# Performance work log

Hardware: AMD Instinct MI355X
Metric: run time of the kernel (lower is better)

## Reference

```python
import jax, jax.numpy as jnp
import numpy as np

DIM = 1024
HEADS = 16
DIM_HEAD = 64
INNER = HEADS * DIM_HEAD  # 1024
EPS = 1e-5


def setup_inputs() -> dict:
    key = jax.random.key(0)
    ks = jax.random.split(key, 8)
    B, N = 4, 2048
    s = 0.02
    return {
        "query": jax.random.normal(ks[0], (B, N, DIM), jnp.float32),
        "key_": jax.random.normal(ks[1], (B, N, DIM), jnp.float32),
        "value": jax.random.normal(ks[2], (B, N, DIM), jnp.float32),
        "Wq": jax.random.normal(ks[3], (DIM, INNER), jnp.float32) * s,
        "Wk": jax.random.normal(ks[4], (DIM, INNER), jnp.float32) * s,
        "Wv": jax.random.normal(ks[5], (DIM, INNER), jnp.float32) * s,
        "Wo": jax.random.normal(ks[6], (INNER, DIM), jnp.float32) * s,
        "bo": jnp.zeros((DIM,), jnp.float32),
        "gamma": jnp.ones((DIM,), jnp.float32),
        "beta": jnp.zeros((DIM,), jnp.float32),
    }


def reference(query, key_, value, Wq, Wk, Wv, Wo, bo, gamma, beta):
    B, N, _ = query.shape
    scale = DIM_HEAD ** (-0.5)
    # project and split heads: [B, H, N, Dh]
    q = (query @ Wq).reshape(B, N, HEADS, DIM_HEAD).transpose(0, 2, 1, 3)
    k = (key_ @ Wk).reshape(B, N, HEADS, DIM_HEAD).transpose(0, 2, 1, 3)
    v = (value @ Wv).reshape(B, N, HEADS, DIM_HEAD).transpose(0, 2, 1, 3)
    dots = jnp.einsum("bhnd,bhmd->bhnm", q, k) * scale  # [B,H,N,N]
    attn = jax.nn.softmax(dots, axis=-1)
    out = jnp.einsum("bhnm,bhmd->bhnd", attn, v)
    out = out.transpose(0, 2, 1, 3).reshape(B, N, INNER)
    out = out @ Wo + bo  # dropout p=0.0 is identity
    # LayerNorm over last dim
    mu = out.mean(-1, keepdims=True)
    var = ((out - mu) ** 2).mean(-1, keepdims=True)
    normed = (out - mu) * jax.lax.rsqrt(var + EPS) * gamma + beta
    return normed + query
```

## Files before the change

kernel.cpp:

```cpp
#include <hip/hip_runtime.h>
#include <stdint.h>

#define K_DIM 1024
#define B_SZ 4
#define N_SEQ 2048
#define HEADS 16
#define DH 64
#define M_TOT (B_SZ * N_SEQ)

typedef __bf16 bf16x8 __attribute__((ext_vector_type(8)));
typedef __bf16 bf16x4 __attribute__((ext_vector_type(4)));
typedef float f32x4 __attribute__((ext_vector_type(4)));
typedef short s16x4 __attribute__((ext_vector_type(4)));

typedef const uint32_t __attribute__((address_space(1))) gas_u32;
typedef uint32_t __attribute__((address_space(3))) las_u32;

#define CE_SCALE 0.1803368801f

__device__ __forceinline__ uint16_t f2bf(float f) {
  uint32_t u = __float_as_uint(f);
  u += 0x7FFFu + ((u >> 16) & 1u);
  return (uint16_t)(u >> 16);
}

__device__ __forceinline__ void gld_lds16(const uint16_t* g, uint16_t* lds) {
  __builtin_amdgcn_global_load_lds((gas_u32*)g, (las_u32*)lds, 16, 0, 0);
}

#if defined(__has_builtin)
#if __has_builtin(__builtin_amdgcn_mfma_f32_16x16x16bf16_1k)
#define HAVE_MFMA16_BUILTIN 1
#endif
#endif

__device__ __forceinline__ f32x4 mfma16(bf16x4 a, bf16x4 b, f32x4 c) {
#ifdef HAVE_MFMA16_BUILTIN
  return __builtin_amdgcn_mfma_f32_16x16x16bf16_1k(
      __builtin_bit_cast(s16x4, a), __builtin_bit_cast(s16x4, b), c, 0, 0, 0);
#else
  f32x4 d;
  asm("v_mfma_f32_16x16x16_bf16 %0, %1, %2, %3"
      : "=v"(d)
      : "v"(a), "v"(b), "v"(c));
  return d;
#endif
}

__global__ __launch_bounds__(256) void conv_bf16_k(const float* __restrict__ s0,
                                                   const float* __restrict__ s1,
                                                   const float* __restrict__ s2,
                                                   uint16_t* __restrict__ dstbase, int n4) {
  const int z = blockIdx.y;
  const float* src = (z == 0) ? s0 : (z == 1) ? s1 : s2;
  uint16_t* dst = dstbase + (size_t)z * M_TOT * K_DIM;
  int i = blockIdx.x * blockDim.x + threadIdx.x;
  if (i < n4) {
    float4 v = ((const float4*)src)[i];
    ushort4 o;
    o.x = f2bf(v.x); o.y = f2bf(v.y); o.z = f2bf(v.z); o.w = f2bf(v.w);
    ((ushort4*)dst)[i] = o;
  }
}

__global__ __launch_bounds__(256) void transpose_conv(const float* __restrict__ s0,
                                                      const float* __restrict__ s1,
                                                      const float* __restrict__ s2,
                                                      const float* __restrict__ s3,
                                                      uint16_t* __restrict__ dstbase) {
  __shared__ float tile[32][33];
  const int z = blockIdx.z;
  const float* src = (z == 0) ? s0 : (z == 1) ? s1 : (z == 2) ? s2 : s3;
  uint16_t* dst = dstbase + (size_t)z * 1024 * 1024;
  const int tx = threadIdx.x, ty = threadIdx.y;
  const int bx = blockIdx.x * 32, by = blockIdx.y * 32;
#pragma unroll
  for (int i = 0; i < 32; i += 8)
    tile[ty + i][tx] = src[(size_t)(by + ty + i) * 1024 + bx + tx];
  __syncthreads();
#pragma unroll
  for (int i = 0; i < 32; i += 8)
    dst[(size_t)(bx + ty + i) * 1024 + by + tx] = f2bf(tile[tx][ty + i]);
}

template <int MODE>
__global__ __launch_bounds__(256, 2) void gemm_bf16(const uint16_t* __restrict__ A,
                                                    const uint16_t* __restrict__ BT,
                                                    void* __restrict__ Cout,
                                                    const float* __restrict__ bias) {
  __shared__ __align__(16) uint16_t As[128 * 32];
  __shared__ __align__(16) uint16_t Bs[128 * 32];
  const int tid = threadIdx.x;
  const int wave = tid >> 6, lane = tid & 63;
  const int g = lane >> 4, c16 = lane & 15;

  const int bid = blockIdx.x;
  const int xcd = bid & 7;
  const int l = bid >> 3;
  const int z = (MODE == 3) ? (l >> 6) : 0;
  const int r = l & 63;
  const int n0 = (r & 7) * 128;
  const int m0 = (xcd * 8 + (r >> 3)) * 128;

  const int wr = wave >> 1, wc = wave & 1;
  float scale = 1.f;
  if (MODE == 3) {
    A += (size_t)z * M_TOT * K_DIM;
    BT += (size_t)z * 1024 * 1024;
    scale = (z == 0) ? CE_SCALE : 1.f;
  }

  const f32x4 fzero = {0.f, 0.f, 0.f, 0.f};
  f32x4 acc[4][4];
#pragma unroll
  for (int i = 0; i < 4; ++i)
#pragma unroll
    for (int j = 0; j < 4; ++j) acc[i][j] = fzero;

  const int srow = wave * 32 + (lane >> 2);
  const int scol = (lane & 3) * 8;
  const uint16_t* ag0 = A + (size_t)(m0 + srow) * K_DIM + scol;
  const uint16_t* ag1 = A + (size_t)(m0 + srow + 16) * K_DIM + scol;
  const uint16_t* bg0 = BT + (size_t)(n0 + srow) * K_DIM + scol;
  const uint16_t* bg1 = BT + (size_t)(n0 + srow + 16) * K_DIM + scol;
  uint16_t* la0 = &As[(wave * 32) * 32];
  uint16_t* la1 = &As[(wave * 32 + 16) * 32];
  uint16_t* lb0 = &Bs[(wave * 32) * 32];
  uint16_t* lb1 = &Bs[(wave * 32 + 16) * 32];

  for (int kt = 0; kt < K_DIM / 32; ++kt) {
    __syncthreads();
    gld_lds16(ag0 + kt * 32, la0);
    gld_lds16(ag1 + kt * 32, la1);
    gld_lds16(bg0 + kt * 32, lb0);
    gld_lds16(bg1 + kt * 32, lb1);
    __syncthreads();
    bf16x8 avec[4], bvec[4];
#pragma unroll
    for (int i = 0; i < 4; ++i)
      avec[i] = *(const bf16x8*)&As[(wr * 64 + i * 16 + c16) * 32 + g * 8];
#pragma unroll
    for (int j = 0; j < 4; ++j)
      bvec[j] = *(const bf16x8*)&Bs[(wc * 64 + j * 16 + c16) * 32 + g * 8];
#pragma unroll
    for (int i = 0; i < 4; ++i)
#pragma unroll
      for (int j = 0; j < 4; ++j)
        acc[i][j] = __builtin_amdgcn_mfma_f32_16x16x32_bf16(avec[i], bvec[j], acc[i][j], 0, 0, 0);
  }

#pragma unroll
  for (int i = 0; i < 4; ++i) {
#pragma unroll
    for (int j = 0; j < 4; ++j) {
      const int col = n0 + wc * 64 + j * 16 + c16;
      if (MODE == 3 && z == 2) {
        const int h = col >> 6, d = col & 63;
        const int row0 = m0 + wr * 64 + i * 16 + g * 4;
        const int b = row0 >> 11, n = row0 & 2047;
        ushort4 o;
        o.x = f2bf(acc[i][j][0]); o.y = f2bf(acc[i][j][1]);
        o.z = f2bf(acc[i][j][2]); o.w = f2bf(acc[i][j][3]);
        *(ushort4*)&((uint16_t*)Cout)[(size_t)2 * M_TOT * 1024 +
                                      (((size_t)(b * HEADS + h)) * DH + d) * N_SEQ + n] = o;
      } else {
#pragma unroll
        for (int r2 = 0; r2 < 4; ++r2) {
          const int row = m0 + wr * 64 + i * 16 + g * 4 + r2;
          if (MODE == 3) {
            const int b = row >> 11, n = row & 2047;
            const int h = col >> 6, d = col & 63;
            ((uint16_t*)Cout)[(size_t)z * M_TOT * 1024 +
                              (((size_t)(b * HEADS + h)) * N_SEQ + n) * DH + d] =
                f2bf(acc[i][j][r2] * scale);
          } else {
            ((float*)Cout)[(size_t)row * 1024 + col] = acc[i][j][r2] + bias[col];
          }
        }
      }
    }
  }
}

__global__ __launch_bounds__(256, 2) void attention_k(const uint16_t* __restrict__ qm,
                                                      const uint16_t* __restrict__ km,
                                                      const uint16_t* __restrict__ vtm,
                                                      uint16_t* __restrict__ om) {
  __shared__ __align__(16) uint16_t Ks[64 * 64];
  __shared__ __align__(16) uint16_t Vs[64 * 64];
  const int tid = threadIdx.x;
  const int wave = tid >> 6, lane = tid & 63;
  const int g = lane >> 4, c16 = lane & 15;

  const int bid = blockIdx.x;
  const int xcd = bid & 7;
  const int l0 = bid >> 3;
  const int bh = xcd * 8 + (l0 & 7);
  const int qblk = l0 >> 3;
  const int b = bh >> 4, h = bh & 15;
  const int q0 = qblk * 256 + wave * 64;

  const uint16_t* qbase = qm + (size_t)bh * N_SEQ * DH;
  const uint16_t* kbase = km + (size_t)bh * N_SEQ * DH;
  const uint16_t* vbase = vtm + (size_t)bh * DH * N_SEQ;

  bf16x8 qf[4][2];
#pragma unroll
  for (int qc = 0; qc < 4; ++qc) {
    const uint16_t* qp = qbase + (size_t)(q0 + qc * 16 + c16) * DH + g * 8;
    qf[qc][0] = *(const bf16x8*)qp;
    qf[qc][1] = *(const bf16x8*)(qp + 32);
  }

  const f32x4 fz = {0.f, 0.f, 0.f, 0.f};
  f32x4 oacc[4][4];
#pragma unroll
  for (int qc = 0; qc < 4; ++qc)
#pragma unroll
    for (int jt = 0; jt < 4; ++jt) oacc[qc][jt] = fz;
  float l[4] = {0.f, 0.f, 0.f, 0.f};

  const int sw = c16 & 7;

  const int ch = tid & 7;
  const int krow0 = tid >> 3, krow1 = (256 + tid) >> 3;
  const int kdst0 = krow0 * 64 + ((ch ^ (krow0 & 7)) << 3);
  const int kdst1 = krow1 * 64 + ((ch ^ (krow1 & 7)) << 3);

  uint4 kp0, kp1, vp0, vp1;
  kp0 = *(const uint4*)&kbase[(size_t)tid * 8];
  kp1 = *(const uint4*)&kbase[(size_t)(256 + tid) * 8];
  vp0 = *(const uint4*)&vbase[(size_t)krow0 * N_SEQ + ch * 8];
  vp1 = *(const uint4*)&vbase[(size_t)krow1 * N_SEQ + ch * 8];
  *(uint4*)&Ks[kdst0] = kp0;
  *(uint4*)&Ks[kdst1] = kp1;
  *(uint4*)&Vs[kdst0] = vp0;
  *(uint4*)&Vs[kdst1] = vp1;
  __syncthreads();

  for (int t = 0; t < N_SEQ / 64; ++t) {
    if (t < N_SEQ / 64 - 1) {
      const size_t ko = (size_t)(t + 1) * 4096;
      const int vc = (t + 1) * 64;
      kp0 = *(const uint4*)&kbase[ko + (size_t)tid * 8];
      kp1 = *(const uint4*)&kbase[ko + (size_t)(256 + tid) * 8];
      vp0 = *(const uint4*)&vbase[(size_t)krow0 * N_SEQ + vc + ch * 8];
      vp1 = *(const uint4*)&vbase[(size_t)krow1 * N_SEQ + vc + ch * 8];
    }

#pragma unroll
    for (int kt = 0; kt < 4; ++kt) {
      const int krow = kt * 16 + c16;
      bf16x8 kf0 = *(const bf16x8*)&Ks[krow * 64 + ((g ^ sw) << 3)];
      bf16x8 kf1 = *(const bf16x8*)&Ks[krow * 64 + (((4 + g) ^ sw) << 3)];
      bf16x4 pk[4];
#pragma unroll
      for (int qc = 0; qc < 4; ++qc) {
        f32x4 z = fz;
        z = __builtin_amdgcn_mfma_f32_16x16x32_bf16(kf0, qf[qc][0], z, 0, 0, 0);
        z = __builtin_amdgcn_mfma_f32_16x16x32_bf16(kf1, qf[qc][1], z, 0, 0, 0);
        const float p0 = __builtin_amdgcn_exp2f(z[0]);
        const float p1 = __builtin_amdgcn_exp2f(z[1]);
        const float p2 = __builtin_amdgcn_exp2f(z[2]);
        const float p3 = __builtin_amdgcn_exp2f(z[3]);
        l[qc] += (p0 + p1) + (p2 + p3);
        bf16x4 pq;
        pq[0] = (__bf16)p0; pq[1] = (__bf16)p1; pq[2] = (__bf16)p2; pq[3] = (__bf16)p3;
        pk[qc] = pq;
      }
#pragma unroll
      for (int jt = 0; jt < 4; ++jt) {
        bf16x4 vb = *(const bf16x4*)&Vs[(jt * 16 + c16) * 64 +
                                        (((kt * 2 + (g >> 1)) ^ sw) << 3) + (g & 1) * 4];
#pragma unroll
        for (int qc = 0; qc < 4; ++qc) oacc[qc][jt] = mfma16(pk[qc], vb, oacc[qc][jt]);
      }
    }

    if (t < N_SEQ / 64 - 1) {
      __syncthreads();
      *(uint4*)&Ks[kdst0] = kp0;
      *(uint4*)&Ks[kdst1] = kp1;
      *(uint4*)&Vs[kdst0] = vp0;
      *(uint4*)&Vs[kdst1] = vp1;
      __syncthreads();
    }
  }

#pragma unroll
  for (int qc = 0; qc < 4; ++qc) {
    l[qc] += __shfl_xor(l[qc], 16);
    l[qc] += __shfl_xor(l[qc], 32);
  }

#pragma unroll
  for (int qc = 0; qc < 4; ++qc) {
#pragma unroll
    for (int r = 0; r < 4; ++r) {
      const float lr = __shfl(l[qc], g * 4 + r, 16);
      const float inv = 1.f / lr;
      const int row = q0 + qc * 16 + g * 4 + r;
      const size_t base = ((size_t)b * N_SEQ + row) * 1024 + h * 64;
#pragma unroll
      for (int jt = 0; jt < 4; ++jt)
        om[base + jt * 16 + c16] = f2bf(oacc[qc][jt][r] * inv);
    }
  }
}

__global__ __launch_bounds__(256) void ln_res_k(const float* __restrict__ proj,
                                                const float* __restrict__ query,
                                                const float* __restrict__ gamma,
                                                const float* __restrict__ beta,
                                                float* __restrict__ out) {
  const int row = blockIdx.x;
  const int tid = threadIdx.x;
  const size_t base = (size_t)row * 1024 + tid * 4;
  float4 v = *(const float4*)(proj + base);
  float s = v.x + v.y + v.z + v.w;
  float s2 = v.x * v.x + v.y * v.y + v.z * v.z + v.w * v.w;
#pragma unroll
  for (int off = 1; off < 64; off <<= 1) {
    s += __shfl_xor(s, off);
    s2 += __shfl_xor(s2, off);
  }
  __shared__ float red[8];
  const int wave = tid >> 6, lane = tid & 63;
  if (lane == 0) { red[wave] = s; red[4 + wave] = s2; }
  __syncthreads();
  s = red[0] + red[1] + red[2] + red[3];
  s2 = red[4] + red[5] + red[6] + red[7];
  const float mu = s * (1.f / 1024.f);
  const float var = fmaxf(s2 * (1.f / 1024.f) - mu * mu, 0.f);
  const float rstd = rsqrtf(var + 1e-5f);
  float4 gq = *(const float4*)(gamma + tid * 4);
  float4 bq = *(const float4*)(beta + tid * 4);
  float4 qq = *(const float4*)(query + base);
  float4 o;
  o.x = (v.x - mu) * rstd * gq.x + bq.x + qq.x;
  o.y = (v.y - mu) * rstd * gq.y + bq.y + qq.y;
  o.z = (v.z - mu) * rstd * gq.z + bq.z + qq.z;
  o.w = (v.w - mu) * rstd * gq.w + bq.w + qq.w;
  *(float4*)(out + base) = o;
}

extern "C" void kernel_launch(void* const* d_in, const int* in_sizes, int n_in,
                              void* d_out, int out_size, void* d_ws, size_t ws_size,
                              hipStream_t stream) {
  (void)in_sizes; (void)n_in; (void)out_size; (void)ws_size;
  const float* query = (const float*)d_in[0];
  const float* key_ = (const float*)d_in[1];
  const float* value = (const float*)d_in[2];
  const float* Wq = (const float*)d_in[3];
  const float* Wk = (const float*)d_in[4];
  const float* Wv = (const float*)d_in[5];
  const float* Wo = (const float*)d_in[6];
  const float* bo = (const float*)d_in[7];
  const float* gamma = (const float*)d_in[8];
  const float* beta = (const float*)d_in[9];
  float* out = (float*)d_out;

  const size_t NELEM = (size_t)M_TOT * 1024;
  uint16_t* wsp = (uint16_t*)d_ws;
  uint16_t* WqT = wsp;
  uint16_t* WoT = WqT + 3 * 1024 * 1024;
  uint16_t* xq = WqT + 4 * 1024 * 1024;
  uint16_t* qb = xq + 3 * NELEM;
  uint16_t* attnO = xq;
  float* proj = (float*)(xq + NELEM);

  const int n4 = (int)(NELEM / 4);
  conv_bf16_k<<<dim3(8192, 3), 256, 0, stream>>>(query, key_, value, xq, n4);

  transpose_conv<<<dim3(32, 32, 4), dim3(32, 8), 0, stream>>>(Wq, Wk, Wv, Wo, WqT);

  gemm_bf16<3><<<1536, 256, 0, stream>>>(xq, WqT, qb, nullptr);

  attention_k<<<512, 256, 0, stream>>>(qb, qb + NELEM, qb + 2 * NELEM, attnO);

  gemm_bf16<1><<<512, 256, 0, stream>>>(attnO, WoT, proj, bo);

  ln_res_k<<<8192, 256, 0, stream>>>(proj, query, gamma, beta, out);
}
```

Baseline: 346.1 us.

## Double-buffer K/V tiles and use 8 waves of 32 query rows in attention

The attention kernel now launches 512 threads per block, with each wave handling 32 query rows instead of 64. K/V tiles in shared memory are double-buffered, so each iteration needs one barrier instead of two, and every thread stages a single 16-byte chunk of K and V. The aim is more waves for latency hiding and less synchronisation stall. In exchange each wave holds fewer accumulators, so every K/V LDS fragment feeds half as many MFMAs, and shared-memory use per block doubles.

```diff
diff --git a/kernel.cpp b/kernel.cpp
--- a/kernel.cpp
+++ b/kernel.cpp
@@ -182,12 +182,12 @@
   }
 }
 
-__global__ __launch_bounds__(256, 2) void attention_k(const uint16_t* __restrict__ qm,
+__global__ __launch_bounds__(512, 4) void attention_k(const uint16_t* __restrict__ qm,
                                                       const uint16_t* __restrict__ km,
                                                       const uint16_t* __restrict__ vtm,
                                                       uint16_t* __restrict__ om) {
-  __shared__ __align__(16) uint16_t Ks[64 * 64];
-  __shared__ __align__(16) uint16_t Vs[64 * 64];
+  __shared__ __align__(16) uint16_t Ks[2 * 64 * 64];
+  __shared__ __align__(16) uint16_t Vs[2 * 64 * 64];
   const int tid = threadIdx.x;
   const int wave = tid >> 6, lane = tid & 63;
   const int g = lane >> 4, c16 = lane & 15;
@@ -198,64 +198,61 @@
   const int bh = xcd * 8 + (l0 & 7);
   const int qblk = l0 >> 3;
   const int b = bh >> 4, h = bh & 15;
-  const int q0 = qblk * 256 + wave * 64;
+  const int q0 = qblk * 256 + wave * 32;
 
   const uint16_t* qbase = qm + (size_t)bh * N_SEQ * DH;
   const uint16_t* kbase = km + (size_t)bh * N_SEQ * DH;
   const uint16_t* vbase = vtm + (size_t)bh * DH * N_SEQ;
 
-  bf16x8 qf[4][2];
-#pragma unroll
-  for (int qc = 0; qc < 4; ++qc) {
+  bf16x8 qf[2][2];
+#pragma unroll
+  for (int qc = 0; qc < 2; ++qc) {
     const uint16_t* qp = qbase + (size_t)(q0 + qc * 16 + c16) * DH + g * 8;
     qf[qc][0] = *(const bf16x8*)qp;
     qf[qc][1] = *(const bf16x8*)(qp + 32);
   }
 
   const f32x4 fz = {0.f, 0.f, 0.f, 0.f};
-  f32x4 oacc[4][4];
-#pragma unroll
-  for (int qc = 0; qc < 4; ++qc)
+  f32x4 oacc[2][4];
+#pragma unroll
+  for (int qc = 0; qc < 2; ++qc)
 #pragma unroll
     for (int jt = 0; jt < 4; ++jt) oacc[qc][jt] = fz;
-  float l[4] = {0.f, 0.f, 0.f, 0.f};
+  float l[2] = {0.f, 0.f};
 
   const int sw = c16 & 7;
 
   const int ch = tid & 7;
-  const int krow0 = tid >> 3, krow1 = (256 + tid) >> 3;
-  const int kdst0 = krow0 * 64 + ((ch ^ (krow0 & 7)) << 3);
-  const int kdst1 = krow1 * 64 + ((ch ^ (krow1 & 7)) << 3);
-
-  uint4 kp0, kp1, vp0, vp1;
-  kp0 = *(const uint4*)&kbase[(size_t)tid * 8];
-  kp1 = *(const uint4*)&kbase[(size_t)(256 + tid) * 8];
-  vp0 = *(const uint4*)&vbase[(size_t)krow0 * N_SEQ + ch * 8];
-  vp1 = *(const uint4*)&vbase[(size_t)krow1 * N_SEQ + ch * 8];
-  *(uint4*)&Ks[kdst0] = kp0;
-  *(uint4*)&Ks[kdst1] = kp1;
-  *(uint4*)&Vs[kdst0] = vp0;
-  *(uint4*)&Vs[kdst1] = vp1;
+  const int srow = tid >> 3;
+  const int kdst = srow * 64 + ((ch ^ (srow & 7)) << 3);
+
+  uint4 kp, vp;
+  kp = *(const uint4*)&kbase[(size_t)tid * 8];
+  vp = *(const uint4*)&vbase[(size_t)srow * N_SEQ + ch * 8];
+  *(uint4*)&Ks[kdst] = kp;
+  *(uint4*)&Vs[kdst] = vp;
   __syncthreads();
 
   for (int t = 0; t < N_SEQ / 64; ++t) {
+    const int cur = t & 1;
     if (t < N_SEQ / 64 - 1) {
       const size_t ko = (size_t)(t + 1) * 4096;
       const int vc = (t + 1) * 64;
-      kp0 = *(const uint4*)&kbase[ko + (size_t)tid * 8];
-      kp1 = *(const uint4*)&kbase[ko + (size_t)(256 + tid) * 8];
-      vp0 = *(const uint4*)&vbase[(size_t)krow0 * N_SEQ + vc + ch * 8];
-      vp1 = *(const uint4*)&vbase[(size_t)krow1 * N_SEQ + vc + ch * 8];
-    }
+      kp = *(const uint4*)&kbase[ko + (size_t)tid * 8];
+      vp = *(const uint4*)&vbase[(size_t)srow * N_SEQ + vc + ch * 8];
+    }
+
+    const uint16_t* ks = &Ks[cur * 4096];
+    const uint16_t* vs = &Vs[cur * 4096];
 
 #pragma unroll
     for (int kt = 0; kt < 4; ++kt) {
       const int krow = kt * 16 + c16;
-      bf16x8 kf0 = *(const bf16x8*)&Ks[krow * 64 + ((g ^ sw) << 3)];
-      bf16x8 kf1 = *(const bf16x8*)&Ks[krow * 64 + (((4 + g) ^ sw) << 3)];
-      bf16x4 pk[4];
-#pragma unroll
-      for (int qc = 0; qc < 4; ++qc) {
+      bf16x8 kf0 = *(const bf16x8*)&ks[krow * 64 + ((g ^ sw) << 3)];
+      bf16x8 kf1 = *(const bf16x8*)&ks[krow * 64 + (((4 + g) ^ sw) << 3)];
+      bf16x4 pk[2];
+#pragma unroll
+      for (int qc = 0; qc < 2; ++qc) {
         f32x4 z = fz;
         z = __builtin_amdgcn_mfma_f32_16x16x32_bf16(kf0, qf[qc][0], z, 0, 0, 0);
         z = __builtin_amdgcn_mfma_f32_16x16x32_bf16(kf1, qf[qc][1], z, 0, 0, 0);
@@ -270,31 +267,28 @@
       }
 #pragma unroll
       for (int jt = 0; jt < 4; ++jt) {
-        bf16x4 vb = *(const bf16x4*)&Vs[(jt * 16 + c16) * 64 +
+        bf16x4 vb = *(const bf16x4*)&vs[(jt * 16 + c16) * 64 +
                                         (((kt * 2 + (g >> 1)) ^ sw) << 3) + (g & 1) * 4];
 #pragma unroll
-        for (int qc = 0; qc < 4; ++qc) oacc[qc][jt] = mfma16(pk[qc], vb, oacc[qc][jt]);
+        for (int qc = 0; qc < 2; ++qc) oacc[qc][jt] = mfma16(pk[qc], vb, oacc[qc][jt]);
       }
     }
 
     if (t < N_SEQ / 64 - 1) {
+      *(uint4*)&Ks[(cur ^ 1) * 4096 + kdst] = kp;
+      *(uint4*)&Vs[(cur ^ 1) * 4096 + kdst] = vp;
       __syncthreads();
-      *(uint4*)&Ks[kdst0] = kp0;
-      *(uint4*)&Ks[kdst1] = kp1;
-      *(uint4*)&Vs[kdst0] = vp0;
-      *(uint4*)&Vs[kdst1] = vp1;
-      __syncthreads();
-    }
-  }
-
-#pragma unroll
-  for (int qc = 0; qc < 4; ++qc) {
+    }
+  }
+
+#pragma unroll
+  for (int qc = 0; qc < 2; ++qc) {
     l[qc] += __shfl_xor(l[qc], 16);
     l[qc] += __shfl_xor(l[qc], 32);
   }
 
 #pragma unroll
-  for (int qc = 0; qc < 4; ++qc) {
+  for (int qc = 0; qc < 2; ++qc) {
 #pragma unroll
     for (int r = 0; r < 4; ++r) {
       const float lr = __shfl(l[qc], g * 4 + r, 16);
@@ -376,7 +370,7 @@
 
   gemm_bf16<3><<<1536, 256, 0, stream>>>(xq, WqT, qb, nullptr);
 
-  attention_k<<<512, 256, 0, stream>>>(qb, qb + NELEM, qb + 2 * NELEM, attnO);
+  attention_k<<<512, 512, 0, stream>>>(qb, qb + NELEM, qb + 2 * NELEM, attnO);
 
   gemm_bf16<1><<<512, 256, 0, stream>>>(attnO, WoT, proj, bo);
 
```

After: 348.7 us. Within noise of the previous version (+0.7%).

## Switch attention kernel to 32x32x16 MFMA with permlane-swapped P and double-buffered LDS

Applied to the files above, without the earlier changes.

Restructures the attention inner loop to use 32x32x16 bf16 MFMA tiles for both QK^T and PV. The P fragments are repacked in registers with v_permlane32_swap so they can feed the second MFMA directly. K/V shared-memory tiles are double-buffered, which removes one barrier per iteration, and setprio hints are added around the MFMA bursts. The aim is fewer MFMA and LDS instructions per FLOP and less sync overhead, at the cost of more registers and LDS, which may reduce occupancy.

```diff
diff --git a/kernel.cpp b/kernel.cpp
--- a/kernel.cpp
+++ b/kernel.cpp
@@ -10,8 +10,9 @@
 
 typedef __bf16 bf16x8 __attribute__((ext_vector_type(8)));
 typedef __bf16 bf16x4 __attribute__((ext_vector_type(4)));
+typedef __bf16 bf16x2 __attribute__((ext_vector_type(2)));
 typedef float f32x4 __attribute__((ext_vector_type(4)));
-typedef short s16x4 __attribute__((ext_vector_type(4)));
+typedef float f32x16 __attribute__((ext_vector_type(16)));
 
 typedef const uint32_t __attribute__((address_space(1))) gas_u32;
 typedef uint32_t __attribute__((address_space(3))) las_u32;
@@ -28,23 +29,15 @@
   __builtin_amdgcn_global_load_lds((gas_u32*)g, (las_u32*)lds, 16, 0, 0);
 }
 
-#if defined(__has_builtin)
-#if __has_builtin(__builtin_amdgcn_mfma_f32_16x16x16bf16_1k)
-#define HAVE_MFMA16_BUILTIN 1
-#endif
-#endif
-
-__device__ __forceinline__ f32x4 mfma16(bf16x4 a, bf16x4 b, f32x4 c) {
-#ifdef HAVE_MFMA16_BUILTIN
-  return __builtin_amdgcn_mfma_f32_16x16x16bf16_1k(
-      __builtin_bit_cast(s16x4, a), __builtin_bit_cast(s16x4, b), c, 0, 0, 0);
-#else
-  f32x4 d;
-  asm("v_mfma_f32_16x16x16_bf16 %0, %1, %2, %3"
-      : "=v"(d)
-      : "v"(a), "v"(b), "v"(c));
-  return d;
-#endif
+__device__ __forceinline__ uint32_t pkbf(float a, float b) {
+  bf16x2 t;
+  t[0] = (__bf16)a;
+  t[1] = (__bf16)b;
+  return __builtin_bit_cast(uint32_t, t);
+}
+
+__device__ __forceinline__ void pswap(uint32_t& a, uint32_t& b) {
+  asm("v_permlane32_swap_b32 %0, %1" : "+v"(a), "+v"(b));
 }
 
 __global__ __launch_bounds__(256) void conv_bf16_k(const float* __restrict__ s0,
@@ -186,11 +179,12 @@
                                                       const uint16_t* __restrict__ km,
                                                       const uint16_t* __restrict__ vtm,
                                                       uint16_t* __restrict__ om) {
-  __shared__ __align__(16) uint16_t Ks[64 * 64];
-  __shared__ __align__(16) uint16_t Vs[64 * 64];
+  __shared__ __align__(16) uint16_t Ks[2 * 64 * 64];
+  __shared__ __align__(16) uint16_t Vs[2 * 64 * 64];
   const int tid = threadIdx.x;
   const int wave = tid >> 6, lane = tid & 63;
-  const int g = lane >> 4, c16 = lane & 15;
+  const int lrow = lane & 31;
+  const int hi = lane >> 5;
 
   const int bid = blockIdx.x;
   const int xcd = bid & 7;
@@ -198,32 +192,47 @@
   const int bh = xcd * 8 + (l0 & 7);
   const int qblk = l0 >> 3;
   const int b = bh >> 4, h = bh & 15;
-  const int q0 = qblk * 256 + wave * 64;
+  const int q0w = qblk * 256 + wave * 64;
 
   const uint16_t* qbase = qm + (size_t)bh * N_SEQ * DH;
   const uint16_t* kbase = km + (size_t)bh * N_SEQ * DH;
   const uint16_t* vbase = vtm + (size_t)bh * DH * N_SEQ;
 
-  bf16x8 qf[4][2];
-#pragma unroll
-  for (int qc = 0; qc < 4; ++qc) {
-    const uint16_t* qp = qbase + (size_t)(q0 + qc * 16 + c16) * DH + g * 8;
-    qf[qc][0] = *(const bf16x8*)qp;
-    qf[qc][1] = *(const bf16x8*)(qp + 32);
-  }
-
-  const f32x4 fz = {0.f, 0.f, 0.f, 0.f};
-  f32x4 oacc[4][4];
-#pragma unroll
-  for (int qc = 0; qc < 4; ++qc)
-#pragma unroll
-    for (int jt = 0; jt < 4; ++jt) oacc[qc][jt] = fz;
-  float l[4] = {0.f, 0.f, 0.f, 0.f};
-
-  const int sw = c16 & 7;
+  bf16x8 qf[2][4];
+#pragma unroll
+  for (int qs = 0; qs < 2; ++qs) {
+    const uint16_t* qp = qbase + (size_t)(q0w + qs * 32 + lrow) * DH + hi * 8;
+#pragma unroll
+    for (int step = 0; step < 4; ++step) qf[qs][step] = *(const bf16x8*)(qp + step * 16);
+  }
+
+  int koff[2][4];
+  int voff[2][2][2];
+#pragma unroll
+  for (int ks = 0; ks < 2; ++ks) {
+    const int krow = ks * 32 + lrow;
+#pragma unroll
+    for (int step = 0; step < 4; ++step)
+      koff[ks][step] = krow * 64 + ((((step << 1) | hi) ^ (krow & 7)) << 3);
+#pragma unroll
+    for (int s = 0; s < 2; ++s)
+#pragma unroll
+      for (int dt = 0; dt < 2; ++dt)
+        voff[ks][s][dt] =
+            (dt * 32 + lrow) * 64 + ((((ks << 2) | (s << 1) | hi) ^ (lrow & 7)) << 3);
+  }
+
+  f32x16 oacc[2][2];
+#pragma unroll
+  for (int qs = 0; qs < 2; ++qs)
+#pragma unroll
+    for (int dt = 0; dt < 2; ++dt)
+#pragma unroll
+      for (int i = 0; i < 16; ++i) oacc[qs][dt][i] = 0.f;
+  float l[2] = {0.f, 0.f};
 
   const int ch = tid & 7;
-  const int krow0 = tid >> 3, krow1 = (256 + tid) >> 3;
+  const int krow0 = tid >> 3, krow1 = 32 + (tid >> 3);
   const int kdst0 = krow0 * 64 + ((ch ^ (krow0 & 7)) << 3);
   const int kdst1 = krow1 * 64 + ((ch ^ (krow1 & 7)) << 3);
 
@@ -239,6 +248,7 @@
   __syncthreads();
 
   for (int t = 0; t < N_SEQ / 64; ++t) {
+    const int cur = t & 1;
     if (t < N_SEQ / 64 - 1) {
       const size_t ko = (size_t)(t + 1) * 4096;
       const int vc = (t + 1) * 64;
@@ -247,63 +257,93 @@
       vp0 = *(const uint4*)&vbase[(size_t)krow0 * N_SEQ + vc + ch * 8];
       vp1 = *(const uint4*)&vbase[(size_t)krow1 * N_SEQ + vc + ch * 8];
     }
-
-#pragma unroll
-    for (int kt = 0; kt < 4; ++kt) {
-      const int krow = kt * 16 + c16;
-      bf16x8 kf0 = *(const bf16x8*)&Ks[krow * 64 + ((g ^ sw) << 3)];
-      bf16x8 kf1 = *(const bf16x8*)&Ks[krow * 64 + (((4 + g) ^ sw) << 3)];
-      bf16x4 pk[4];
-#pragma unroll
-      for (int qc = 0; qc < 4; ++qc) {
-        f32x4 z = fz;
-        z = __builtin_amdgcn_mfma_f32_16x16x32_bf16(kf0, qf[qc][0], z, 0, 0, 0);
-        z = __builtin_amdgcn_mfma_f32_16x16x32_bf16(kf1, qf[qc][1], z, 0, 0, 0);
-        const float p0 = __builtin_amdgcn_exp2f(z[0]);
-        const float p1 = __builtin_amdgcn_exp2f(z[1]);
-        const float p2 = __builtin_amdgcn_exp2f(z[2]);
-        const float p3 = __builtin_amdgcn_exp2f(z[3]);
-        l[qc] += (p0 + p1) + (p2 + p3);
-        bf16x4 pq;
-        pq[0] = (__bf16)p0; pq[1] = (__bf16)p1; pq[2] = (__bf16)p2; pq[3] = (__bf16)p3;
-        pk[qc] = pq;
+    const uint16_t* ksp = &Ks[cur * 4096];
+    const uint16_t* vsp = &Vs[cur * 4096];
+
+#pragma unroll
+    for (int ks = 0; ks < 2; ++ks) {
+      bf16x8 kf[4];
+#pragma unroll
+      for (int step = 0; step < 4; ++step) kf[step] = *(const bf16x8*)&ksp[koff[ks][step]];
+
+      f32x16 z[2];
+#pragma unroll
+      for (int qs = 0; qs < 2; ++qs)
+#pragma unroll
+        for (int i = 0; i < 16; ++i) z[qs][i] = 0.f;
+
+      __builtin_amdgcn_s_setprio(1);
+#pragma unroll
+      for (int step = 0; step < 4; ++step)
+        z[0] = __builtin_amdgcn_mfma_f32_32x32x16_bf16(kf[step], qf[0][step], z[0], 0, 0, 0);
+#pragma unroll
+      for (int step = 0; step < 4; ++step)
+        z[1] = __builtin_amdgcn_mfma_f32_32x32x16_bf16(kf[step], qf[1][step], z[1], 0, 0, 0);
+      __builtin_amdgcn_s_setprio(0);
+
+      uint32_t pa[2][2][4];
+#pragma unroll
+      for (int qs = 0; qs < 2; ++qs) {
+        float p[16];
+#pragma unroll
+        for (int r = 0; r < 16; ++r) p[r] = __builtin_amdgcn_exp2f(z[qs][r]);
+        l[qs] += (((p[0] + p[1]) + (p[2] + p[3])) + ((p[4] + p[5]) + (p[6] + p[7]))) +
+                 (((p[8] + p[9]) + (p[10] + p[11])) + ((p[12] + p[13]) + (p[14] + p[15])));
+#pragma unroll
+        for (int s = 0; s < 2; ++s) {
+          uint32_t w0 = pkbf(p[s * 8 + 0], p[s * 8 + 1]);
+          uint32_t w1 = pkbf(p[s * 8 + 2], p[s * 8 + 3]);
+          uint32_t w2 = pkbf(p[s * 8 + 4], p[s * 8 + 5]);
+          uint32_t w3 = pkbf(p[s * 8 + 6], p[s * 8 + 7]);
+          pswap(w0, w2);
+          pswap(w1, w3);
+          pa[qs][s][0] = w0; pa[qs][s][1] = w1; pa[qs][s][2] = w2; pa[qs][s][3] = w3;
+        }
       }
-#pragma unroll
-      for (int jt = 0; jt < 4; ++jt) {
-        bf16x4 vb = *(const bf16x4*)&Vs[(jt * 16 + c16) * 64 +
-                                        (((kt * 2 + (g >> 1)) ^ sw) << 3) + (g & 1) * 4];
-#pragma unroll
-        for (int qc = 0; qc < 4; ++qc) oacc[qc][jt] = mfma16(pk[qc], vb, oacc[qc][jt]);
-      }
+
+      bf16x8 vf[2][2];
+#pragma unroll
+      for (int s = 0; s < 2; ++s)
+#pragma unroll
+        for (int dt = 0; dt < 2; ++dt) vf[s][dt] = *(const bf16x8*)&vsp[voff[ks][s][dt]];
+
+      __builtin_amdgcn_s_setprio(1);
+#pragma unroll
+      for (int s = 0; s < 2; ++s)
+#pragma unroll
+        for (int qs = 0; qs < 2; ++qs) {
+          uint4 u;
+          u.x = pa[qs][s][0]; u.y = pa[qs][s][1]; u.z = pa[qs][s][2]; u.w = pa[qs][s][3];
+          const bf16x8 paf = __builtin_bit_cast(bf16x8, u);
+          oacc[qs][0] = __builtin_amdgcn_mfma_f32_32x32x16_bf16(paf, vf[s][0], oacc[qs][0], 0, 0, 0);
+          oacc[qs][1] = __builtin_amdgcn_mfma_f32_32x32x16_bf16(paf, vf[s][1], oacc[qs][1], 0, 0, 0);
+        }
+      __builtin_amdgcn_s_setprio(0);
     }
 
     if (t < N_SEQ / 64 - 1) {
-      __syncthreads();
-      *(uint4*)&Ks[kdst0] = kp0;
-      *(uint4*)&Ks[kdst1] = kp1;
-      *(uint4*)&Vs[kdst0] = vp0;
-      *(uint4*)&Vs[kdst1] = vp1;
+      *(uint4*)&Ks[(cur ^ 1) * 4096 + kdst0] = kp0;
+      *(uint4*)&Ks[(cur ^ 1) * 4096 + kdst1] = kp1;
+      *(uint4*)&Vs[(cur ^ 1) * 4096 + kdst0] = vp0;
+      *(uint4*)&Vs[(cur ^ 1) * 4096 + kdst1] = vp1;
       __syncthreads();
     }
   }
 
 #pragma unroll
-  for (int qc = 0; qc < 4; ++qc) {
-    l[qc] += __shfl_xor(l[qc], 16);
-    l[qc] += __shfl_xor(l[qc], 32);
-  }
-
-#pragma unroll
-  for (int qc = 0; qc < 4; ++qc) {
-#pragma unroll
-    for (int r = 0; r < 4; ++r) {
-      const float lr = __shfl(l[qc], g * 4 + r, 16);
+  for (int qs = 0; qs < 2; ++qs) l[qs] += __shfl_xor(l[qs], 32);
+
+#pragma unroll
+  for (int qs = 0; qs < 2; ++qs) {
+#pragma unroll
+    for (int r = 0; r < 16; ++r) {
+      const int ql = (r & 3) + 8 * (r >> 2) + 4 * hi;
+      const float lr = __shfl(l[qs], ql);
       const float inv = 1.f / lr;
-      const int row = q0 + qc * 16 + g * 4 + r;
+      const int row = q0w + qs * 32 + ql;
       const size_t base = ((size_t)b * N_SEQ + row) * 1024 + h * 64;
-#pragma unroll
-      for (int jt = 0; jt < 4; ++jt)
-        om[base + jt * 16 + c16] = f2bf(oacc[qc][jt][r] * inv);
+      om[base + lrow] = f2bf(oacc[qs][0][r] * inv);
+      om[base + 32 + lrow] = f2bf(oacc[qs][1][r] * inv);
     }
   }
 }
```

Measured after the change: 341.7 us. No clear change (-1.3%).
